# Kernel optimization log

Hardware: AMD Instinct MI355X
Metric: run time of the kernel (lower is better)

Reference implementation:

```python
import jax, jax.numpy as jnp
import numpy as np

B, S, E = 4, 2048, 1024
H, DK = 16, 64

def setup_inputs() -> dict:
    key = jax.random.key(0)
    ks = jax.random.split(key, 9)
    sc = 1.0 / np.sqrt(E)
    return {
        "q": jax.random.normal(ks[0], (B, S, E), jnp.float32),
        "Wq": jax.random.normal(ks[1], (E, H * DK), jnp.float32) * sc,
        "bq": jax.random.normal(ks[2], (H * DK,), jnp.float32) * 0.01,
        "Wk": jax.random.normal(ks[3], (E, H * DK), jnp.float32) * sc,
        "bk": jax.random.normal(ks[4], (H * DK,), jnp.float32) * 0.01,
        "Wv": jax.random.normal(ks[5], (E, H * DK), jnp.float32) * sc,
        "bv": jax.random.normal(ks[6], (H * DK,), jnp.float32) * 0.01,
        "Wo": jax.random.normal(ks[7], (H * DK, E), jnp.float32) * sc,
        "bo": jax.random.normal(ks[8], (E,), jnp.float32) * 0.01,
    }

def _split_heads(x):
    # (B, S, H*DK) -> (B, H, S, DK)
    return x.reshape(B, S, H, DK).transpose(0, 2, 1, 3)

def reference(q, Wq, bq, Wk, bk, Wv, bv, Wo, bo):
    # self-attention: k = v = q (torch module path when k=v=None)
    qh = _split_heads(q @ Wq + bq)
    kh = _split_heads(q @ Wk + bk)
    vh = _split_heads(q @ Wv + bv)
    scale = 1.0 / jnp.sqrt(jnp.asarray(DK, qh.dtype))
    scores = jnp.einsum("bhqd,bhkd->bhqk", qh, kh) * scale  # (B,H,S,S)
    attn = jax.nn.softmax(scores, axis=-1)
    ctx = jnp.einsum("bhqk,bhkd->bhqd", attn, vh)
    ctx = ctx.transpose(0, 2, 1, 3).reshape(B, S, H * DK)
    return ctx @ Wo + bo
```

## Files before the change

### kernel.cpp

```cpp
#include <hip/hip_runtime.h>
#include <hip/hip_bf16.h>
#include <math.h>


typedef _Float16 f16x8 __attribute__((ext_vector_type(8)));
typedef _Float16 f16x4 __attribute__((ext_vector_type(4)));
typedef _Float16 f16x2 __attribute__((ext_vector_type(2)));
typedef float    f32x4 __attribute__((ext_vector_type(4)));

#define MFMA16(a,b,c) __builtin_amdgcn_mfma_f32_16x16x32_f16(a,b,c,0,0,0)

__device__ __forceinline__ void async_cp16(const _Float16* g, _Float16* l) {
    __builtin_amdgcn_global_load_lds(
        (const __attribute__((address_space(1))) unsigned int*)g,
        (__attribute__((address_space(3))) unsigned int*)l,
        16, 0, 0);
}

__device__ __forceinline__ f16x2 pk(float a, float b) {
    return __builtin_bit_cast(f16x2, __builtin_amdgcn_cvt_pkrtz(a, b));
}

__global__ void __launch_bounds__(256) prep_weights(
    const float* __restrict__ Wq, const float* __restrict__ Wk,
    const float* __restrict__ Wv, const float* __restrict__ Wo,
    _Float16* __restrict__ wt)
{
    __shared__ float tile[32][33];
    int mat = blockIdx.y;
    const float* W = (mat==0)?Wq:(mat==1)?Wk:(mat==2)?Wv:Wo;
    _Float16* WT = wt + (size_t)mat*1048576;
    int t = blockIdx.x;
    int kb = (t & 31) * 32;
    int nb = (t >> 5) * 32;
    int tx = threadIdx.x & 31, ty = threadIdx.x >> 5;
    #pragma unroll
    for (int r = 0; r < 4; ++r) {
        int row = ty + r*8;
        tile[row][tx] = W[(size_t)(kb+row)*1024 + nb + tx];
    }
    __syncthreads();
    #pragma unroll
    for (int r = 0; r < 4; ++r) {
        int row = ty + r*8;
        WT[(size_t)(nb+row)*1024 + kb + tx] = (_Float16)tile[tx][row];
    }
}

__global__ void __launch_bounds__(256) cvt_x(
    const float* __restrict__ X, _Float16* __restrict__ Xh)
{
    int i = (blockIdx.x*256 + threadIdx.x)*4;
    f32x4 x = *(const f32x4*)&X[i];
    f16x4 h;
    #pragma unroll
    for (int k=0;k<4;k++) h[k] = (_Float16)x[k];
    *(f16x4*)&Xh[i] = h;
}

__global__ void __launch_bounds__(256) gemm_qkv(
    const _Float16* __restrict__ Xh, const _Float16* __restrict__ wt,
    const float* __restrict__ bq, const float* __restrict__ bk, const float* __restrict__ bv,
    _Float16* __restrict__ Q, _Float16* __restrict__ K, _Float16* __restrict__ Vt)
{
    __shared__ __align__(16) _Float16 sA[8192];
    __shared__ __align__(16) _Float16 sB[8192];

    const int id = blockIdx.x;
    const int msub = id & 7;
    const int t2 = id >> 3;
    const int nblk = t2 % 24;
    const int mblk = (t2 / 24) * 8 + msub;

    const int tid = threadIdx.x;
    const int wave = tid >> 6, lane = tid & 63;
    const int wr = wave >> 1, wc = wave & 1;
    const int q4 = lane >> 4, cc = lane & 15;

    const int mat = nblk >> 3;
    const int colbase = (nblk & 7) * 128;
    const _Float16* Bg = wt + (size_t)mat*1048576 + (size_t)colbase*1024;
    const _Float16* Ag = Xh + (size_t)mblk*131072;

    f32x4 acc[4][4] = {};

    const int srow = tid >> 3;
    const int scg  = ((tid & 7) ^ ((tid >> 3) & 7)) * 8;

    for (int kb = 0; kb < 1024; kb += 64) {
        __syncthreads();
        #pragma unroll
        for (int rr = 0; rr < 4; ++rr) {
            async_cp16(&Ag[(size_t)(rr*32 + srow)*1024 + kb + scg], sA + rr*2048 + wave*512);
            async_cp16(&Bg[(size_t)(rr*32 + srow)*1024 + kb + scg], sB + rr*2048 + wave*512);
        }
        __syncthreads();
        #pragma unroll
        for (int ks = 0; ks < 2; ++ks) {
            f16x8 af[4], bf[4];
            #pragma unroll
            for (int i=0;i<4;i++){
                af[i] = *(const f16x8*)&sA[(wr*64+i*16+cc)*64 + ((ks*4+q4)^(cc&7))*8];
                bf[i] = *(const f16x8*)&sB[(wc*64+i*16+cc)*64 + ((ks*4+q4)^(cc&7))*8];
            }
            #pragma unroll
            for (int i=0;i<4;i++)
                #pragma unroll
                for (int j=0;j<4;j++)
                    acc[i][j] = MFMA16(af[i], bf[j], acc[i][j]);
        }
    }

    const float* bias = (mat==0)?bq:(mat==1)?bk:bv;
    const float QSCALE = 0.125f * 1.44269504f;
    #pragma unroll
    for (int i=0;i<4;i++)
      #pragma unroll
      for (int j=0;j<4;j++)
        #pragma unroll
        for (int r=0;r<4;r++){
            int m = mblk*128 + wr*64 + i*16 + q4*4 + r;
            int ncol = colbase + wc*64 + j*16 + cc;
            float val = acc[i][j][r] + bias[ncol];
            int b = m >> 11, s = m & 2047;
            int h = ncol >> 6, dk = ncol & 63;
            if (mat == 2) {
                Vt[((size_t)(b*16+h)*64 + dk)*2048 + s] = (_Float16)val;
            } else {
                size_t qi = ((size_t)(b*16+h)*2048 + s)*64 + dk;
                if (mat == 0) Q[qi] = (_Float16)(val * QSCALE);
                else          K[qi] = (_Float16)val;
            }
        }
}

__global__ void __launch_bounds__(256,2) attn(
    const _Float16* __restrict__ Qg, const _Float16* __restrict__ Kg,
    const _Float16* __restrict__ Vg,
    _Float16* __restrict__ Ctx)
{
    __shared__ __align__(16) _Float16 sK[128][72];
    __shared__ __align__(16) _Float16 sV[64][136];
    __shared__ __align__(16) _Float16 sP[128*128];

    const int id = blockIdx.x;
    const int xcd = id & 7;
    const int t2 = id >> 3;
    const int qc = t2 & 15;
    const int bh = (t2 >> 4) * 8 + xcd;

    const int tid = threadIdx.x;
    const int wave = tid >> 6, lane = tid & 63;
    const int q4 = lane >> 4, cc = lane & 15;

    const size_t hoff = (size_t)bh * 131072;
    const _Float16* Qp = Qg + hoff;
    const _Float16* Kp = Kg + hoff;
    const _Float16* Vp = Vg + hoff;

    const int qbase = qc*128 + wave*32;

    f16x8 qf[2][2];
    #pragma unroll
    for (int m=0;m<2;m++)
      #pragma unroll
      for (int ks=0;ks<2;ks++)
        qf[m][ks] = *(const f16x8*)&Qp[(qbase+m*16+cc)*64 + ks*32 + q4*8];

    f16x8 vones;
    #pragma unroll
    for (int k=0;k<8;k++) vones[k] = (_Float16)1.0f;

    f32x4 o[2][4] = {};
    f32x4 oL[2] = {};

    const int r0 = tid >> 3, c8 = (tid & 7)*8;
    const int vrow = tid >> 4, vg = (tid & 15)*8;

    const int prow_w0 = wave*32 + cc;

    f16x8 kr[4], vr[4];
    #pragma unroll
    for (int p=0;p<4;p++){
        kr[p] = *(const f16x8*)&Kp[(p*32 + r0)*64 + c8];
        vr[p] = *(const f16x8*)&Vp[(size_t)(p*16 + vrow)*2048 + vg];
    }

    for (int kt = 0; kt < 16; ++kt) {
        __syncthreads();
        #pragma unroll
        for (int p=0;p<4;p++){
            *(f16x8*)&sK[p*32+r0][c8] = kr[p];
            *(f16x8*)&sV[p*16+vrow][vg] = vr[p];
        }
        __syncthreads();
        if (kt < 15) {
            #pragma unroll
            for (int p=0;p<4;p++){
                kr[p] = *(const f16x8*)&Kp[((kt+1)*128 + p*32 + r0)*64 + c8];
                vr[p] = *(const f16x8*)&Vp[(size_t)(p*16 + vrow)*2048 + (kt+1)*128 + vg];
            }
        }

        #pragma unroll
        for (int kj=0;kj<8;kj++){
            f16x8 k0 = *(const f16x8*)&sK[kj*16+cc][q4*8];
            f16x8 k1 = *(const f16x8*)&sK[kj*16+cc][32+q4*8];
            #pragma unroll
            for (int m=0;m<2;m++){
                f32x4 z = {};
                f32x4 s = MFMA16(k0, qf[m][0], z);
                s = MFMA16(k1, qf[m][1], s);
                float p0 = __builtin_amdgcn_exp2f(s[0]);
                float p1 = __builtin_amdgcn_exp2f(s[1]);
                float p2 = __builtin_amdgcn_exp2f(s[2]);
                float p3 = __builtin_amdgcn_exp2f(s[3]);
                union { f16x4 v4; f16x2 v2[2]; } u;
                u.v2[0] = pk(p0, p1);
                u.v2[1] = pk(p2, p3);
                int row = prow_w0 + m*16;
                int g   = (kj*2 + (q4>>1)) ^ (row & 7);
                *(f16x4*)&sP[row*128 + g*8 + (q4&1)*4] = u.v4;
            }
        }

        #pragma unroll
        for (int ks=0;ks<4;ks++){
            int g0 = ks*4 + q4;
            int row0 = prow_w0;
            int row1 = prow_w0 + 16;
            f16x8 p0 = *(const f16x8*)&sP[row0*128 + (g0 ^ (row0 & 7))*8];
            f16x8 p1 = *(const f16x8*)&sP[row1*128 + (g0 ^ (row1 & 7))*8];
            #pragma unroll
            for (int v=0;v<4;v++){
                f16x8 vf = *(const f16x8*)&sV[v*16+cc][ks*32+q4*8];
                o[0][v] = MFMA16(p0, vf, o[0][v]);
                o[1][v] = MFMA16(p1, vf, o[1][v]);
            }
            oL[0] = MFMA16(p0, vones, oL[0]);
            oL[1] = MFMA16(p1, vones, oL[1]);
        }
    }

    int b = bh >> 4, h = bh & 15;
    #pragma unroll
    for (int m=0;m<2;m++)
      #pragma unroll
      for (int r=0;r<4;r++){
        float inv = 1.f / oL[m][r];
        int s = qbase + m*16 + q4*4 + r;
        #pragma unroll
        for (int v=0;v<4;v++){
            float val = o[m][v][r]*inv;
            int dk = v*16 + cc;
            Ctx[((size_t)(b*2048+s)*16 + h)*64 + dk] = (_Float16)val;
        }
      }
}

__global__ void __launch_bounds__(256) gemm_out(
    const _Float16* __restrict__ Ctx, const _Float16* __restrict__ wt,
    const float* __restrict__ bo,
    float* __restrict__ out)
{
    __shared__ __align__(16) _Float16 sA[8192];
    __shared__ __align__(16) _Float16 sB[8192];

    const int id = blockIdx.x;
    const int msub = id & 7;
    const int t2 = id >> 3;
    const int nblk = t2 & 7;
    const int mblk = (t2 >> 3) * 8 + msub;

    const int tid = threadIdx.x;
    const int wave = tid >> 6, lane = tid & 63;
    const int wr = wave >> 1, wc = wave & 1;
    const int q4 = lane >> 4, cc = lane & 15;

    const _Float16* Bg = wt + (size_t)3*1048576 + (size_t)nblk*128*1024;
    const _Float16* Ag = Ctx + (size_t)mblk*131072;

    f32x4 acc[4][4] = {};
    const int srow = tid >> 3;
    const int scg  = ((tid & 7) ^ ((tid >> 3) & 7)) * 8;

    for (int kb = 0; kb < 1024; kb += 64) {
        __syncthreads();
        #pragma unroll
        for (int rr = 0; rr < 4; ++rr) {
            async_cp16(&Ag[(size_t)(rr*32 + srow)*1024 + kb + scg], sA + rr*2048 + wave*512);
            async_cp16(&Bg[(size_t)(rr*32 + srow)*1024 + kb + scg], sB + rr*2048 + wave*512);
        }
        __syncthreads();
        #pragma unroll
        for (int ks = 0; ks < 2; ++ks) {
            f16x8 af[4], bf[4];
            #pragma unroll
            for (int i=0;i<4;i++){
                af[i] = *(const f16x8*)&sA[(wr*64+i*16+cc)*64 + ((ks*4+q4)^(cc&7))*8];
                bf[i] = *(const f16x8*)&sB[(wc*64+i*16+cc)*64 + ((ks*4+q4)^(cc&7))*8];
            }
            #pragma unroll
            for (int i=0;i<4;i++)
                #pragma unroll
                for (int j=0;j<4;j++)
                    acc[i][j] = MFMA16(af[i], bf[j], acc[i][j]);
        }
    }

    #pragma unroll
    for (int i=0;i<4;i++)
      #pragma unroll
      for (int j=0;j<4;j++)
        #pragma unroll
        for (int r=0;r<4;r++){
            int m = mblk*128 + wr*64 + i*16 + q4*4 + r;
            int n = nblk*128 + wc*64 + j*16 + cc;
            out[(size_t)m*1024 + n] = acc[i][j][r] + bo[n];
        }
}

extern "C" void kernel_launch(void* const* d_in, const int* in_sizes, int n_in,
                              void* d_out, int out_size, void* d_ws, size_t ws_size,
                              hipStream_t stream)
{
    const float* q  = (const float*)d_in[0];
    const float* Wq = (const float*)d_in[1];
    const float* bq = (const float*)d_in[2];
    const float* Wk = (const float*)d_in[3];
    const float* bk = (const float*)d_in[4];
    const float* Wv = (const float*)d_in[5];
    const float* bv = (const float*)d_in[6];
    const float* Wo = (const float*)d_in[7];
    const float* bo = (const float*)d_in[8];
    float* out = (float*)d_out;

    _Float16* ws  = (_Float16*)d_ws;
    _Float16* wt  = ws;
    _Float16* Xh  = ws + 4194304;
    _Float16* Q   = ws + 12582912;
    _Float16* K   = ws + 20971520;
    _Float16* Vt  = ws + 29360128;
    _Float16* Ctx = Xh;

    prep_weights<<<dim3(1024,4), 256, 0, stream>>>(Wq, Wk, Wv, Wo, wt);
    cvt_x<<<dim3(8192), 256, 0, stream>>>(q, Xh);
    gemm_qkv<<<dim3(1536), 256, 0, stream>>>(Xh, wt, bq, bk, bv, Q, K, Vt);
    attn<<<dim3(1024), 256, 0, stream>>>(Q, K, Vt, Ctx);
    gemm_out<<<dim3(512), 256, 0, stream>>>(Ctx, wt, bo, out);
}
```

Before: 300.8 us.

## Double-buffer GEMM LDS tiles via register prefetch; load K directly to registers in attention

Both projection GEMMs stop using direct global-to-LDS async copies. They now stage the next K-slab in registers and write it into a second LDS buffer, so each iteration needs only one barrier and global loads overlap the MFMA work. The attention kernel drops the shared K tile. Each lane loads its MFMA K fragments straight from global memory and prefetches the next tile after the QK/exp phase, which also removes the 2-blocks-per-SM launch bound. This raises register and LDS use, which may lower occupancy, and K is now read without coalesced LDS staging.

```diff
diff --git a/kernel.cpp b/kernel.cpp
--- a/kernel.cpp
+++ b/kernel.cpp
@@ -9,13 +9,6 @@
 typedef float    f32x4 __attribute__((ext_vector_type(4)));
 
 #define MFMA16(a,b,c) __builtin_amdgcn_mfma_f32_16x16x32_f16(a,b,c,0,0,0)
-
-__device__ __forceinline__ void async_cp16(const _Float16* g, _Float16* l) {
-    __builtin_amdgcn_global_load_lds(
-        (const __attribute__((address_space(1))) unsigned int*)g,
-        (__attribute__((address_space(3))) unsigned int*)l,
-        16, 0, 0);
-}
 
 __device__ __forceinline__ f16x2 pk(float a, float b) {
     return __builtin_bit_cast(f16x2, __builtin_amdgcn_cvt_pkrtz(a, b));
@@ -63,8 +56,8 @@
     const float* __restrict__ bq, const float* __restrict__ bk, const float* __restrict__ bv,
     _Float16* __restrict__ Q, _Float16* __restrict__ K, _Float16* __restrict__ Vt)
 {
-    __shared__ __align__(16) _Float16 sA[8192];
-    __shared__ __align__(16) _Float16 sB[8192];
+    __shared__ __align__(16) _Float16 sA[2][8192];
+    __shared__ __align__(16) _Float16 sB[2][8192];
 
     const int id = blockIdx.x;
     const int msub = id & 7;
@@ -87,21 +80,48 @@
     const int srow = tid >> 3;
     const int scg  = ((tid & 7) ^ ((tid >> 3) & 7)) * 8;
 
-    for (int kb = 0; kb < 1024; kb += 64) {
+    f16x8 ra[4], rb[4];
+    #pragma unroll
+    for (int rr=0; rr<4; ++rr) {
+        ra[rr] = *(const f16x8*)&Ag[(size_t)(rr*32+srow)*1024 + scg];
+        rb[rr] = *(const f16x8*)&Bg[(size_t)(rr*32+srow)*1024 + scg];
+    }
+    #pragma unroll
+    for (int rr=0; rr<4; ++rr) {
+        *(f16x8*)&sA[0][rr*2048 + tid*8] = ra[rr];
+        *(f16x8*)&sB[0][rr*2048 + tid*8] = rb[rr];
+    }
+    #pragma unroll
+    for (int rr=0; rr<4; ++rr) {
+        ra[rr] = *(const f16x8*)&Ag[(size_t)(rr*32+srow)*1024 + 64 + scg];
+        rb[rr] = *(const f16x8*)&Bg[(size_t)(rr*32+srow)*1024 + 64 + scg];
+    }
+
+    int cur = 0;
+    for (int it = 0; it < 16; ++it) {
         __syncthreads();
-        #pragma unroll
-        for (int rr = 0; rr < 4; ++rr) {
-            async_cp16(&Ag[(size_t)(rr*32 + srow)*1024 + kb + scg], sA + rr*2048 + wave*512);
-            async_cp16(&Bg[(size_t)(rr*32 + srow)*1024 + kb + scg], sB + rr*2048 + wave*512);
-        }
-        __syncthreads();
+        if (it < 15) {
+            #pragma unroll
+            for (int rr=0; rr<4; ++rr) {
+                *(f16x8*)&sA[cur^1][rr*2048 + tid*8] = ra[rr];
+                *(f16x8*)&sB[cur^1][rr*2048 + tid*8] = rb[rr];
+            }
+            if (it < 14) {
+                int kb = (it+2)*64;
+                #pragma unroll
+                for (int rr=0; rr<4; ++rr) {
+                    ra[rr] = *(const f16x8*)&Ag[(size_t)(rr*32+srow)*1024 + kb + scg];
+                    rb[rr] = *(const f16x8*)&Bg[(size_t)(rr*32+srow)*1024 + kb + scg];
+                }
+            }
+        }
         #pragma unroll
         for (int ks = 0; ks < 2; ++ks) {
             f16x8 af[4], bf[4];
             #pragma unroll
             for (int i=0;i<4;i++){
-                af[i] = *(const f16x8*)&sA[(wr*64+i*16+cc)*64 + ((ks*4+q4)^(cc&7))*8];
-                bf[i] = *(const f16x8*)&sB[(wc*64+i*16+cc)*64 + ((ks*4+q4)^(cc&7))*8];
+                af[i] = *(const f16x8*)&sA[cur][(wr*64+i*16+cc)*64 + ((ks*4+q4)^(cc&7))*8];
+                bf[i] = *(const f16x8*)&sB[cur][(wc*64+i*16+cc)*64 + ((ks*4+q4)^(cc&7))*8];
             }
             #pragma unroll
             for (int i=0;i<4;i++)
@@ -109,6 +129,7 @@
                 for (int j=0;j<4;j++)
                     acc[i][j] = MFMA16(af[i], bf[j], acc[i][j]);
         }
+        cur ^= 1;
     }
 
     const float* bias = (mat==0)?bq:(mat==1)?bk:bv;
@@ -134,12 +155,11 @@
         }
 }
 
-__global__ void __launch_bounds__(256,2) attn(
+__global__ void __launch_bounds__(256) attn(
     const _Float16* __restrict__ Qg, const _Float16* __restrict__ Kg,
     const _Float16* __restrict__ Vg,
     _Float16* __restrict__ Ctx)
 {
-    __shared__ __align__(16) _Float16 sK[128][72];
     __shared__ __align__(16) _Float16 sV[64][136];
     __shared__ __align__(16) _Float16 sP[128*128];
 
@@ -174,43 +194,41 @@
     f32x4 o[2][4] = {};
     f32x4 oL[2] = {};
 
-    const int r0 = tid >> 3, c8 = (tid & 7)*8;
     const int vrow = tid >> 4, vg = (tid & 15)*8;
 
     const int prow_w0 = wave*32 + cc;
 
-    f16x8 kr[4], vr[4];
-    #pragma unroll
-    for (int p=0;p<4;p++){
-        kr[p] = *(const f16x8*)&Kp[(p*32 + r0)*64 + c8];
+    f16x8 vr[4];
+    #pragma unroll
+    for (int p=0;p<4;p++)
         vr[p] = *(const f16x8*)&Vp[(size_t)(p*16 + vrow)*2048 + vg];
+
+    f16x8 kf[8][2];
+    #pragma unroll
+    for (int kj=0;kj<8;kj++){
+        kf[kj][0] = *(const f16x8*)&Kp[(size_t)(kj*16+cc)*64 + q4*8];
+        kf[kj][1] = *(const f16x8*)&Kp[(size_t)(kj*16+cc)*64 + 32 + q4*8];
     }
 
     for (int kt = 0; kt < 16; ++kt) {
         __syncthreads();
         #pragma unroll
-        for (int p=0;p<4;p++){
-            *(f16x8*)&sK[p*32+r0][c8] = kr[p];
+        for (int p=0;p<4;p++)
             *(f16x8*)&sV[p*16+vrow][vg] = vr[p];
-        }
         __syncthreads();
         if (kt < 15) {
             #pragma unroll
-            for (int p=0;p<4;p++){
-                kr[p] = *(const f16x8*)&Kp[((kt+1)*128 + p*32 + r0)*64 + c8];
+            for (int p=0;p<4;p++)
                 vr[p] = *(const f16x8*)&Vp[(size_t)(p*16 + vrow)*2048 + (kt+1)*128 + vg];
-            }
         }
 
         #pragma unroll
         for (int kj=0;kj<8;kj++){
-            f16x8 k0 = *(const f16x8*)&sK[kj*16+cc][q4*8];
-            f16x8 k1 = *(const f16x8*)&sK[kj*16+cc][32+q4*8];
             #pragma unroll
             for (int m=0;m<2;m++){
                 f32x4 z = {};
-                f32x4 s = MFMA16(k0, qf[m][0], z);
-                s = MFMA16(k1, qf[m][1], s);
+                f32x4 s = MFMA16(kf[kj][0], qf[m][0], z);
+                s = MFMA16(kf[kj][1], qf[m][1], s);
                 float p0 = __builtin_amdgcn_exp2f(s[0]);
                 float p1 = __builtin_amdgcn_exp2f(s[1]);
                 float p2 = __builtin_amdgcn_exp2f(s[2]);
@@ -224,6 +242,14 @@
             }
         }
 
+        if (kt < 15) {
+            #pragma unroll
+            for (int kj=0;kj<8;kj++){
+                kf[kj][0] = *(const f16x8*)&Kp[(size_t)((kt+1)*128 + kj*16+cc)*64 + q4*8];
+                kf[kj][1] = *(const f16x8*)&Kp[(size_t)((kt+1)*128 + kj*16+cc)*64 + 32 + q4*8];
+            }
+        }
+
         #pragma unroll
         for (int ks=0;ks<4;ks++){
             int g0 = ks*4 + q4;
@@ -263,8 +289,8 @@
     const float* __restrict__ bo,
     float* __restrict__ out)
 {
-    __shared__ __align__(16) _Float16 sA[8192];
-    __shared__ __align__(16) _Float16 sB[8192];
+    __shared__ __align__(16) _Float16 sA[2][8192];
+    __shared__ __align__(16) _Float16 sB[2][8192];
 
     const int id = blockIdx.x;
     const int msub = id & 7;
@@ -284,21 +310,48 @@
     const int srow = tid >> 3;
     const int scg  = ((tid & 7) ^ ((tid >> 3) & 7)) * 8;
 
-    for (int kb = 0; kb < 1024; kb += 64) {
+    f16x8 ra[4], rb[4];
+    #pragma unroll
+    for (int rr=0; rr<4; ++rr) {
+        ra[rr] = *(const f16x8*)&Ag[(size_t)(rr*32+srow)*1024 + scg];
+        rb[rr] = *(const f16x8*)&Bg[(size_t)(rr*32+srow)*1024 + scg];
+    }
+    #pragma unroll
+    for (int rr=0; rr<4; ++rr) {
+        *(f16x8*)&sA[0][rr*2048 + tid*8] = ra[rr];
+        *(f16x8*)&sB[0][rr*2048 + tid*8] = rb[rr];
+    }
+    #pragma unroll
+    for (int rr=0; rr<4; ++rr) {
+        ra[rr] = *(const f16x8*)&Ag[(size_t)(rr*32+srow)*1024 + 64 + scg];
+        rb[rr] = *(const f16x8*)&Bg[(size_t)(rr*32+srow)*1024 + 64 + scg];
+    }
+
+    int cur = 0;
+    for (int it = 0; it < 16; ++it) {
         __syncthreads();
-        #pragma unroll
-        for (int rr = 0; rr < 4; ++rr) {
-            async_cp16(&Ag[(size_t)(rr*32 + srow)*1024 + kb + scg], sA + rr*2048 + wave*512);
-            async_cp16(&Bg[(size_t)(rr*32 + srow)*1024 + kb + scg], sB + rr*2048 + wave*512);
-        }
-        __syncthreads();
+        if (it < 15) {
+            #pragma unroll
+            for (int rr=0; rr<4; ++rr) {
+                *(f16x8*)&sA[cur^1][rr*2048 + tid*8] = ra[rr];
+                *(f16x8*)&sB[cur^1][rr*2048 + tid*8] = rb[rr];
+            }
+            if (it < 14) {
+                int kb = (it+2)*64;
+                #pragma unroll
+                for (int rr=0; rr<4; ++rr) {
+                    ra[rr] = *(const f16x8*)&Ag[(size_t)(rr*32+srow)*1024 + kb + scg];
+                    rb[rr] = *(const f16x8*)&Bg[(size_t)(rr*32+srow)*1024 + kb + scg];
+                }
+            }
+        }
         #pragma unroll
         for (int ks = 0; ks < 2; ++ks) {
             f16x8 af[4], bf[4];
             #pragma unroll
             for (int i=0;i<4;i++){
-                af[i] = *(const f16x8*)&sA[(wr*64+i*16+cc)*64 + ((ks*4+q4)^(cc&7))*8];
-                bf[i] = *(const f16x8*)&sB[(wc*64+i*16+cc)*64 + ((ks*4+q4)^(cc&7))*8];
+                af[i] = *(const f16x8*)&sA[cur][(wr*64+i*16+cc)*64 + ((ks*4+q4)^(cc&7))*8];
+                bf[i] = *(const f16x8*)&sB[cur][(wc*64+i*16+cc)*64 + ((ks*4+q4)^(cc&7))*8];
             }
             #pragma unroll
             for (int i=0;i<4;i++)
@@ -306,6 +359,7 @@
                 for (int j=0;j<4;j++)
                     acc[i][j] = MFMA16(af[i], bf[j], acc[i][j]);
         }
+        cur ^= 1;
     }
 
     #pragma unroll
```

After: 352.9 us. +17.3%, slower.
